# Kernel optimization log

Measured on AMD Instinct MI355X. Metric: run time of the kernel, lower is better.

The kernel has to match this reference:

```python
import jax, jax.numpy as jnp
import numpy as np

N_NODES = 50000
N_EDGES = 1600000
F_IN = 32
F_OUT = 32


def setup_inputs() -> dict:
    key = jax.random.key(0)
    k1, k2, k3, k4, k5 = jax.random.split(key, 5)
    inputs = jax.random.normal(k1, (N_EDGES, F_IN), dtype=jnp.float32)
    src = jax.random.randint(k2, (N_EDGES,), 0, N_NODES, dtype=jnp.int32)
    dst = jax.random.randint(k3, (N_EDGES,), 0, N_NODES, dtype=jnp.int32)
    W = jax.random.normal(k4, (F_OUT, F_IN), dtype=jnp.float32) * (1.0 / np.sqrt(F_IN))
    b = jax.random.normal(k5, (F_OUT,), dtype=jnp.float32) * 0.01
    return {"inputs": inputs, "src": src, "dst": dst, "W": W, "b": b}


def reference(inputs, src, dst, W, b):
    # Step 1: node h = mean of incoming edge features (mean over in-edges).
    ones = jnp.ones((inputs.shape[0],), dtype=inputs.dtype)
    in_deg = jax.ops.segment_sum(ones, dst, num_segments=N_NODES)  # [N]
    node_sum = jax.ops.segment_sum(inputs, dst, num_segments=N_NODES)  # [N, F]
    node_mean = node_sum / jnp.maximum(in_deg, 1.0)[:, None]
    # Step 2: send_and_recv: msg = src node h; reduce = sum at dst node.
    node_h = jax.ops.segment_sum(node_mean[src], dst, num_segments=N_NODES)  # [N, F]
    # Step 3: edge h = mean of its two endpoint node features.
    edge_h = 0.5 * (node_h[src] + node_h[dst])  # [E, F]
    # Step 4: final linear projection on edge features.
    return edge_h @ W.T + b
```

## Files before the change

### kernel.cpp

```cpp
#include <hip/hip_runtime.h>

#define N_NODES 50000
#define N_EDGES 1600000
#define F 32
#define BSH 7
#define BSIZE (1 << BSH)
#define NB ((N_NODES + BSIZE - 1) >> BSH)
#define FILL_CHUNK 4096
#define EMASK 0x1FFFFF

typedef float f4 __attribute__((ext_vector_type(4)));

__device__ __forceinline__ f4 nt_load4(const float* p) {
    return __builtin_nontemporal_load((const f4*)p);
}
__device__ __forceinline__ int nt_loadi(const int* p) {
    return __builtin_nontemporal_load(p);
}

__global__ __launch_bounds__(256)
void k_bhist(const int* __restrict__ dst, int* __restrict__ bhist) {
    __shared__ int lh[NB];
    for (int i = threadIdx.x; i < NB; i += 256) lh[i] = 0;
    __syncthreads();
    for (int e = blockIdx.x * blockDim.x + threadIdx.x; e < N_EDGES;
         e += gridDim.x * blockDim.x)
        atomicAdd(&lh[nt_loadi(&dst[e]) >> BSH], 1);
    __syncthreads();
    for (int i = threadIdx.x; i < NB; i += 256)
        if (lh[i]) atomicAdd(&bhist[i], lh[i]);
}

__global__ __launch_bounds__(512)
void k_bscan(const int* __restrict__ bhist,
             int* __restrict__ bucket_off,
             int* __restrict__ cursor) {
    __shared__ int s[512];
    int t = threadIdx.x;
    int v = (t < NB) ? bhist[t] : 0;
    s[t] = v;
    __syncthreads();
    for (int off = 1; off < 512; off <<= 1) {
        int u = (t >= off) ? s[t - off] : 0;
        __syncthreads();
        s[t] += u;
        __syncthreads();
    }
    if (t < NB) {
        int ex = s[t] - v;
        bucket_off[t] = ex;
        cursor[t] = ex;
    }
    if (t == NB - 1) bucket_off[NB] = s[t];
}

__global__ __launch_bounds__(256)
void k_coarse_fill(const int* __restrict__ dst,
                   const int* __restrict__ src,
                   int* __restrict__ cursor,
                   int* __restrict__ coarseE,
                   unsigned short* __restrict__ coarseS) {
    __shared__ int lh[NB];
    __shared__ int gb[NB];
    int lo = blockIdx.x * FILL_CHUNK;
    int hi = min(lo + FILL_CHUNK, N_EDGES);

    for (int i = threadIdx.x; i < NB; i += 256) lh[i] = 0;
    __syncthreads();
    for (int e = lo + threadIdx.x; e < hi; e += 256)
        atomicAdd(&lh[nt_loadi(&dst[e]) >> BSH], 1);
    __syncthreads();
    for (int i = threadIdx.x; i < NB; i += 256) {
        gb[i] = atomicAdd(&cursor[i], lh[i]);
        lh[i] = 0;
    }
    __syncthreads();
    for (int e = lo + threadIdx.x; e < hi; e += 256) {
        int d = dst[e];
        int bk = d >> BSH;
        int r = atomicAdd(&lh[bk], 1);
        int p = gb[bk] + r;
        coarseE[p] = e | ((d & (BSIZE - 1)) << 21);
        coarseS[p] = (unsigned short)src[e];
    }
}

__global__ __launch_bounds__(256)
void k_exact_fill(const int* __restrict__ coarseE,
                  const unsigned short* __restrict__ coarseS,
                  const int* __restrict__ bucket_off,
                  int* __restrict__ row_off,
                  int* __restrict__ eid_sorted,
                  unsigned short* __restrict__ src_sorted) {
    __shared__ int cnt[BSIZE];
    __shared__ int s[BSIZE];
    __shared__ int cur[BSIZE];
    int tid = threadIdx.x;
    int b = blockIdx.x;
    int lo = bucket_off[b], hi = bucket_off[b + 1];

    if (tid < BSIZE) cnt[tid] = 0;
    __syncthreads();
    for (int i = lo + tid; i < hi; i += 256)
        atomicAdd(&cnt[(coarseE[i] >> 21) & (BSIZE - 1)], 1);
    __syncthreads();
    if (tid < BSIZE) s[tid] = cnt[tid];
    __syncthreads();
    for (int off = 1; off < BSIZE; off <<= 1) {
        int v = 0;
        if (tid < BSIZE && tid >= off) v = s[tid - off];
        __syncthreads();
        if (tid < BSIZE) s[tid] += v;
        __syncthreads();
    }
    int nbase = b << BSH;
    if (tid < BSIZE) {
        int base = lo + s[tid] - cnt[tid];
        cur[tid] = base;
        if (nbase + tid < N_NODES) row_off[nbase + tid] = base;
    }
    if (b == NB - 1 && tid == 0) row_off[N_NODES] = N_EDGES;
    __syncthreads();
    for (int i = lo + tid; i < hi; i += 256) {
        int ev = coarseE[i];
        int l = (ev >> 21) & (BSIZE - 1);
        int p = atomicAdd(&cur[l], 1);
        eid_sorted[p] = ev & EMASK;
        src_sorted[p] = coarseS[i];
    }
}

__global__ __launch_bounds__(256)
void k_node_mean(const float* __restrict__ inputs,
                 const int* __restrict__ eid_sorted,
                 const int* __restrict__ row_off,
                 float* __restrict__ node_mean) {
    int wave = (blockIdx.x * blockDim.x + threadIdx.x) >> 6;
    if (wave >= N_NODES) return;
    int lane  = threadIdx.x & 63;
    int eslot = lane >> 3;
    int q     = lane & 7;

    int s0 = row_off[wave];
    int s1 = row_off[wave + 1];

    f4 acc = {0.f, 0.f, 0.f, 0.f};
    int i = s0 + eslot;
    int e = (i < s1) ? eid_sorted[i] : 0;
    while (i < s1) {
        int inext = i + 8;
        int enext = (inext < s1) ? eid_sorted[inext] : 0;
        f4 v = nt_load4(&inputs[(size_t)e * F + q * 4]);
        acc += v;
        i = inext; e = enext;
    }
    #pragma unroll
    for (int m = 8; m <= 32; m <<= 1) {
        acc.x += __shfl_xor(acc.x, m);
        acc.y += __shfl_xor(acc.y, m);
        acc.z += __shfl_xor(acc.z, m);
        acc.w += __shfl_xor(acc.w, m);
    }
    if (eslot == 0) {
        float r = 1.0f / fmaxf((float)(s1 - s0), 1.0f);
        f4 o = acc * r;
        *reinterpret_cast<f4*>(&node_mean[(size_t)wave * F + q * 4]) = o;
    }
}

__global__ __launch_bounds__(256)
void k_node_h_project(const unsigned short* __restrict__ src_sorted,
                      const int* __restrict__ row_off,
                      const float* __restrict__ node_mean,
                      const float* __restrict__ W,
                      float* __restrict__ node_p) {
    __shared__ float Wl[32][33];
    __shared__ float hr[4][36];

    int tid = threadIdx.x;
    #pragma unroll
    for (int i = tid; i < 1024; i += 256) Wl[i >> 5][i & 31] = W[i];

    int wv    = tid >> 6;
    int lane  = tid & 63;
    int eslot = lane >> 3;
    int q     = lane & 7;
    int n     = blockIdx.x * 4 + wv;

    int s0 = row_off[n];
    int s1 = row_off[n + 1];

    f4 acc = {0.f, 0.f, 0.f, 0.f};
    int i = s0 + eslot;
    int s = (i < s1) ? (int)src_sorted[i] : 0;
    while (i < s1) {
        int inext = i + 8;
        int snext = (inext < s1) ? (int)src_sorted[inext] : 0;
        f4 v = *reinterpret_cast<const f4*>(&node_mean[(size_t)s * F + q * 4]);
        acc += v;
        i = inext; s = snext;
    }
    #pragma unroll
    for (int m = 8; m <= 32; m <<= 1) {
        acc.x += __shfl_xor(acc.x, m);
        acc.y += __shfl_xor(acc.y, m);
        acc.z += __shfl_xor(acc.z, m);
        acc.w += __shfl_xor(acc.w, m);
    }
    if (eslot == 0) {
        *reinterpret_cast<f4*>(&hr[wv][q * 4]) = acc;
    }
    __syncthreads();

    if (tid < 128) {
        int ln = tid >> 5;
        int o  = tid & 31;
        float sacc = 0.f;
        #pragma unroll
        for (int i2 = 0; i2 < 32; ++i2) sacc += hr[ln][i2] * Wl[o][i2];
        node_p[(size_t)(blockIdx.x * 4 + ln) * F + o] = sacc;
    }
}

__global__ __launch_bounds__(256)
void k_edge_out(const int* __restrict__ src,
                const int* __restrict__ dst,
                const float* __restrict__ node_p,
                const float* __restrict__ b,
                float* __restrict__ out) {
    int tid = blockIdx.x * blockDim.x + threadIdx.x;
    if (tid >= N_EDGES * 8) return;
    int e = tid >> 3;
    int q = tid & 7;
    int s = nt_loadi(&src[e]);
    int d = nt_loadi(&dst[e]);

    const f4 a  = *reinterpret_cast<const f4*>(&node_p[(size_t)s * F + q * 4]);
    const f4 c  = *reinterpret_cast<const f4*>(&node_p[(size_t)d * F + q * 4]);
    const f4 bb = *reinterpret_cast<const f4*>(&b[q * 4]);

    f4 r = 0.5f * (a + c) + bb;
    __builtin_nontemporal_store(r, (f4*)&out[(size_t)e * F + q * 4]);
}

extern "C" void kernel_launch(void* const* d_in, const int* in_sizes, int n_in,
                              void* d_out, int out_size, void* d_ws, size_t ws_size,
                              hipStream_t stream) {
    const float* inputs = (const float*)d_in[0];
    const int*   src    = (const int*)d_in[1];
    const int*   dst    = (const int*)d_in[2];
    const float* W      = (const float*)d_in[3];
    const float* b      = (const float*)d_in[4];
    float* out = (float*)d_out;

    float* node_mean = (float*)d_ws;
    float* node_p    = node_mean + (size_t)N_NODES * F;
    int*  coarseE    = (int*)(node_p + (size_t)N_NODES * F);
    int*  eid_sorted = coarseE + N_EDGES;
    int*  bhist      = eid_sorted + N_EDGES;
    int*  bucket_off = bhist + NB;
    int*  cursor     = bucket_off + NB + 1;
    int*  row_off    = cursor + NB;
    unsigned short* coarseS    = (unsigned short*)(row_off + N_NODES + 1);
    unsigned short* src_sorted = coarseS + N_EDGES;

    hipMemsetAsync(bhist, 0, NB * sizeof(int), stream);

    k_bhist<<<256, 256, 0, stream>>>(dst, bhist);
    k_bscan<<<1, 512, 0, stream>>>(bhist, bucket_off, cursor);
    k_coarse_fill<<<(N_EDGES + FILL_CHUNK - 1) / FILL_CHUNK, 256, 0, stream>>>(
        dst, src, cursor, coarseE, coarseS);
    k_exact_fill<<<NB, 256, 0, stream>>>(
        coarseE, coarseS, bucket_off, row_off, eid_sorted, src_sorted);

    int node_blocks = (N_NODES + 3) / 4;
    k_node_mean<<<node_blocks, 256, 0, stream>>>(inputs, eid_sorted, row_off, node_mean);
    k_node_h_project<<<N_NODES / 4, 256, 0, stream>>>(
        src_sorted, row_off, node_mean, W, node_p);
    k_edge_out<<<(N_EDGES * 8 + 255) / 256, 256, 0, stream>>>(src, dst, node_p, b, out);
}
```

Before: 260.4 us.

## Store node_mean and node_p as fp16 to halve gather traffic

```diff
diff --git a/kernel.cpp b/kernel.cpp
--- a/kernel.cpp
+++ b/kernel.cpp
@@ -10,6 +10,7 @@
 #define EMASK 0x1FFFFF
 
 typedef float f4 __attribute__((ext_vector_type(4)));
+typedef _Float16 h4 __attribute__((ext_vector_type(4)));
 
 __device__ __forceinline__ f4 nt_load4(const float* p) {
     return __builtin_nontemporal_load((const f4*)p);
@@ -25,7 +26,7 @@
     __syncthreads();
     for (int e = blockIdx.x * blockDim.x + threadIdx.x; e < N_EDGES;
          e += gridDim.x * blockDim.x)
-        atomicAdd(&lh[nt_loadi(&dst[e]) >> BSH], 1);
+        atomicAdd(&lh[dst[e] >> BSH], 1);
     __syncthreads();
     for (int i = threadIdx.x; i < NB; i += 256)
         if (lh[i]) atomicAdd(&bhist[i], lh[i]);
@@ -68,7 +69,7 @@
     for (int i = threadIdx.x; i < NB; i += 256) lh[i] = 0;
     __syncthreads();
     for (int e = lo + threadIdx.x; e < hi; e += 256)
-        atomicAdd(&lh[nt_loadi(&dst[e]) >> BSH], 1);
+        atomicAdd(&lh[dst[e] >> BSH], 1);
     __syncthreads();
     for (int i = threadIdx.x; i < NB; i += 256) {
         gb[i] = atomicAdd(&cursor[i], lh[i]);
@@ -134,7 +135,7 @@
 void k_node_mean(const float* __restrict__ inputs,
                  const int* __restrict__ eid_sorted,
                  const int* __restrict__ row_off,
-                 float* __restrict__ node_mean) {
+                 _Float16* __restrict__ node_mean) {
     int wave = (blockIdx.x * blockDim.x + threadIdx.x) >> 6;
     if (wave >= N_NODES) return;
     int lane  = threadIdx.x & 63;
@@ -164,16 +165,17 @@
     if (eslot == 0) {
         float r = 1.0f / fmaxf((float)(s1 - s0), 1.0f);
         f4 o = acc * r;
-        *reinterpret_cast<f4*>(&node_mean[(size_t)wave * F + q * 4]) = o;
+        *reinterpret_cast<h4*>(&node_mean[(size_t)wave * F + q * 4]) =
+            __builtin_convertvector(o, h4);
     }
 }
 
 __global__ __launch_bounds__(256)
 void k_node_h_project(const unsigned short* __restrict__ src_sorted,
                       const int* __restrict__ row_off,
-                      const float* __restrict__ node_mean,
+                      const _Float16* __restrict__ node_mean,
                       const float* __restrict__ W,
-                      float* __restrict__ node_p) {
+                      _Float16* __restrict__ node_p) {
     __shared__ float Wl[32][33];
     __shared__ float hr[4][36];
 
@@ -196,8 +198,8 @@
     while (i < s1) {
         int inext = i + 8;
         int snext = (inext < s1) ? (int)src_sorted[inext] : 0;
-        f4 v = *reinterpret_cast<const f4*>(&node_mean[(size_t)s * F + q * 4]);
-        acc += v;
+        h4 v = *reinterpret_cast<const h4*>(&node_mean[(size_t)s * F + q * 4]);
+        acc += __builtin_convertvector(v, f4);
         i = inext; s = snext;
     }
     #pragma unroll
@@ -218,14 +220,14 @@
         float sacc = 0.f;
         #pragma unroll
         for (int i2 = 0; i2 < 32; ++i2) sacc += hr[ln][i2] * Wl[o][i2];
-        node_p[(size_t)(blockIdx.x * 4 + ln) * F + o] = sacc;
+        node_p[(size_t)(blockIdx.x * 4 + ln) * F + o] = (_Float16)sacc;
     }
 }
 
 __global__ __launch_bounds__(256)
 void k_edge_out(const int* __restrict__ src,
                 const int* __restrict__ dst,
-                const float* __restrict__ node_p,
+                const _Float16* __restrict__ node_p,
                 const float* __restrict__ b,
                 float* __restrict__ out) {
     int tid = blockIdx.x * blockDim.x + threadIdx.x;
@@ -235,8 +237,10 @@
     int s = nt_loadi(&src[e]);
     int d = nt_loadi(&dst[e]);
 
-    const f4 a  = *reinterpret_cast<const f4*>(&node_p[(size_t)s * F + q * 4]);
-    const f4 c  = *reinterpret_cast<const f4*>(&node_p[(size_t)d * F + q * 4]);
+    h4 ah = *reinterpret_cast<const h4*>(&node_p[(size_t)s * F + q * 4]);
+    h4 ch = *reinterpret_cast<const h4*>(&node_p[(size_t)d * F + q * 4]);
+    const f4 a  = __builtin_convertvector(ah, f4);
+    const f4 c  = __builtin_convertvector(ch, f4);
     const f4 bb = *reinterpret_cast<const f4*>(&b[q * 4]);
 
     f4 r = 0.5f * (a + c) + bb;
@@ -253,20 +257,20 @@
     const float* b      = (const float*)d_in[4];
     float* out = (float*)d_out;
 
-    float* node_mean = (float*)d_ws;
-    float* node_p    = node_mean + (size_t)N_NODES * F;
-    int*  coarseE    = (int*)(node_p + (size_t)N_NODES * F);
+    int*  coarseE    = (int*)d_ws;
     int*  eid_sorted = coarseE + N_EDGES;
     int*  bhist      = eid_sorted + N_EDGES;
     int*  bucket_off = bhist + NB;
     int*  cursor     = bucket_off + NB + 1;
     int*  row_off    = cursor + NB;
-    unsigned short* coarseS    = (unsigned short*)(row_off + N_NODES + 1);
+    _Float16* node_mean = (_Float16*)(row_off + N_NODES + 1);
+    _Float16* node_p    = node_mean + (size_t)N_NODES * F;
+    unsigned short* coarseS    = (unsigned short*)(node_p + (size_t)N_NODES * F);
     unsigned short* src_sorted = coarseS + N_EDGES;
 
     hipMemsetAsync(bhist, 0, NB * sizeof(int), stream);
 
-    k_bhist<<<256, 256, 0, stream>>>(dst, bhist);
+    k_bhist<<<512, 256, 0, stream>>>(dst, bhist);
     k_bscan<<<1, 512, 0, stream>>>(bhist, bucket_off, cursor);
     k_coarse_fill<<<(N_EDGES + FILL_CHUNK - 1) / FILL_CHUNK, 256, 0, stream>>>(
         dst, src, cursor, coarseE, coarseS);
```

Result: faster. 237.7 us (-8.7%).
